# Performance work log

Measured on AMD Instinct MI355X. Metric: run time of the kernel, lower is better.

Reference implementation:

```python
import math
import jax, jax.numpy as jnp
import numpy as np

B, A, U, S, E, HYP, H = 16384, 32, 64, 2048, 32, 64, 4
ATTEND_REG_COEF = 1e-3


def setup_inputs() -> dict:
    key = jax.random.key(0)
    ks = jax.random.split(key, 12)
    sc = 0.05
    return {
        "agent_qs": jax.random.normal(ks[0], (B, A), jnp.float32),
        "states": jax.random.normal(ks[1], (B, S), jnp.float32),
        # per-head selector hypernet: Linear(S,HYP)+ReLU+Linear(HYP,E,no bias)
        "sel_w1": jax.random.normal(ks[2], (H, S, HYP), jnp.float32) * sc,
        "sel_b1": jax.random.normal(ks[3], (H, HYP), jnp.float32) * sc,
        "sel_w2": jax.random.normal(ks[4], (H, HYP, E), jnp.float32) * sc,
        # per-head key extractor: Linear(U,E,no bias)
        "key_w": jax.random.normal(ks[5], (H, U, E), jnp.float32) * sc,
        # V net: Linear(S,E)+ReLU+Linear(E,1)
        "v_w1": jax.random.normal(ks[6], (S, E), jnp.float32) * sc,
        "v_b1": jax.random.normal(ks[7], (E,), jnp.float32) * sc,
        "v_w2": jax.random.normal(ks[8], (E, 1), jnp.float32) * sc,
        "v_b2": jax.random.normal(ks[9], (1,), jnp.float32) * sc,
    }


def reference(agent_qs, states, sel_w1, sel_b1, sel_w2, key_w, v_w1, v_b1, v_w2, v_b2):
    # nonlinear=False, weighted_head=False, state_bias=True (defaults used here)
    unit_states = states[:, : A * U].reshape(-1, A, U)  # [B, A, U]

    # per-head selectors: [B, H, E]
    h1 = jax.nn.relu(jnp.einsum("bs,hsk->bhk", states, sel_w1) + sel_b1[None])
    selectors = jnp.einsum("bhk,hke->bhe", h1, sel_w2)

    # per-head, per-agent keys: [B, H, A, E]
    keys = jnp.einsum("bau,hue->bhae", unit_states, key_w)

    # attention logits [B, H, A] (matches selector @ stacked-keys in torch)
    logits = jnp.einsum("bhe,bhae->bha", selectors, keys)
    weights = jax.nn.softmax(logits / math.sqrt(E), axis=-1)  # [B, H, A]

    head_attend = jnp.sum(weights, axis=1)  # [B, A]

    v = jax.nn.relu(states @ v_w1 + v_b1) @ v_w2 + v_b2  # [B, 1]

    # coef * sum over heads of mean(logits_h ** 2)
    attend_mag_regs = ATTEND_REG_COEF * jnp.sum(jnp.mean(logits ** 2, axis=(0, 2)))

    # per-head entropy: -(p * log(p + 1e-8)).sum(agents).mean(batch) -> [H]
    head_entropies = -jnp.mean(
        jnp.sum(weights * jnp.log(weights + 1e-8), axis=-1), axis=0
    )

    return head_attend, v, attend_mag_regs, head_entropies
```

## Files before the change

### kernel.cpp

```cpp
#include <hip/hip_runtime.h>
#include <hip/hip_bf16.h>

#define B_N 16384
#define A_N 32
#define U_N 64
#define S_N 2048
#define E_N 32
#define HYP_N 64
#define H_N 4
#define NREAL 288
#define NPADG 320

#define H1B_STRIDE 264

#define WS_WT    0
#define WS_MB    1310720
#define WS_PMAG  (WS_MB + 32768)
#define WS_PENT  (WS_PMAG + 65536)
#define WS_T     (WS_PENT + 262144)
#define WS_HV    (WS_T + 16777216)

#define OUT_V   (B_N * A_N)
#define OUT_MAG (OUT_V + B_N)
#define OUT_ENT (OUT_MAG + 1)

typedef __attribute__((ext_vector_type(8))) short bf16x8_t;
typedef __attribute__((ext_vector_type(4))) float floatx4_t;

#define AS1(p) ((const __attribute__((address_space(1))) void*)(p))
#define AS3(p) ((__attribute__((address_space(3))) void*)(p))

__device__ __forceinline__ unsigned short f2b(float f) {
    union { float f; unsigned u; } v; v.f = f;
    unsigned r = v.u + 0x7FFFu + ((v.u >> 16) & 1u);
    return (unsigned short)(r >> 16);
}
__device__ __forceinline__ float b2f(unsigned x) {
    union { unsigned u; float f; } v; v.u = x << 16; return v.f;
}
__device__ __forceinline__ uint4 pack_bf16x8(float4 a0, float4 a1) {
    uint4 o;
    o.x = (unsigned)f2b(a0.x) | ((unsigned)f2b(a0.y) << 16);
    o.y = (unsigned)f2b(a0.z) | ((unsigned)f2b(a0.w) << 16);
    o.z = (unsigned)f2b(a1.x) | ((unsigned)f2b(a1.y) << 16);
    o.w = (unsigned)f2b(a1.z) | ((unsigned)f2b(a1.w) << 16);
    return o;
}

__global__ __launch_bounds__(256) void pack_w_kernel(
        const float* __restrict__ sel_w1, const float* __restrict__ v_w1,
        const float* __restrict__ sel_w2, const float* __restrict__ key_w,
        unsigned short* __restrict__ Wt, unsigned short* __restrict__ Mb) {
    int idx = blockIdx.x * 256 + threadIdx.x;
    if (idx < NPADG * S_N) {
        int n = idx >> 11;
        int k = idx & 2047;
        float val = 0.0f;
        if (n < 256) {
            int h = n >> 6, kk = n & 63;
            val = sel_w1[((size_t)h * S_N + k) * HYP_N + kk];
        } else if (n < NREAL) {
            val = v_w1[(size_t)k * E_N + (n - 256)];
        }
        Wt[idx] = f2b(val);
    } else if (idx < NPADG * S_N + H_N * U_N * HYP_N) {
        int j = idx - NPADG * S_N;
        int h = j >> 12, u = (j >> 6) & 63, k = j & 63;
        const float* kw = key_w + ((size_t)h * U_N + u) * E_N;
        const float* w2 = sel_w2 + ((size_t)h * HYP_N + k) * E_N;
        float s = 0.0f;
#pragma unroll
        for (int e = 0; e < E_N; ++e) s = fmaf(kw[e], w2[e], s);
        Mb[j] = f2b(s);
    }
}

#define FM_BM 32
#define FM_BK 64
#define NIT   (S_N / FM_BK)

__global__ __launch_bounds__(256, 3) void gemm_t_kernel(
        const float* __restrict__ states, const unsigned short* __restrict__ Wt,
        const float* __restrict__ sel_b1, const float* __restrict__ v_b1,
        const unsigned short* __restrict__ Mb,
        float* __restrict__ tg, unsigned short* __restrict__ hv) {
    __shared__ __align__(16) char pool[4096 + 40960];
    unsigned short* Asm = (unsigned short*)pool;
    unsigned short* Bsm = (unsigned short*)(pool + 4096);
    unsigned short* h1b = (unsigned short*)pool;

    const int t = threadIdx.x;
    const int lane = t & 63;
    const int w = t >> 6;
    const int m0 = blockIdx.x * FM_BM;
    const int nw = w * 80;

    const int ar = t >> 3, acl = t & 7;
    const float* ap = states + (size_t)(m0 + ar) * S_N + acl * 8;
    const int aph = acl ^ (ar & 7);

    floatx4_t acc[2][5] = {};
    float4 a0, a1;

    a0 = *(const float4*)(ap);
    a1 = *(const float4*)(ap + 4);
    *(uint4*)(Asm + (size_t)(ar * 8 + aph) * 8) = pack_bf16x8(a0, a1);
#pragma unroll
    for (int i = 0; i < 10; ++i) {
        int p = i * 256 + t, n = p >> 3, sl = p & 7;
        int cl = sl ^ (n & 7);
        __builtin_amdgcn_global_load_lds(AS1(Wt + (size_t)n * S_N + cl * 8),
                                         AS3(Bsm + p * 8), 16, 0, 0);
    }
    a0 = *(const float4*)(ap + FM_BK);
    a1 = *(const float4*)(ap + FM_BK + 4);
    __syncthreads();

    for (int it = 0; it < NIT; ++it) {
#pragma unroll
        for (int s = 0; s < 2; ++s) {
            const int c = s * 4 + (lane >> 4);
            bf16x8_t afr[2];
#pragma unroll
            for (int mt = 0; mt < 2; ++mt) {
                int r = mt * 16 + (lane & 15);
                afr[mt] = *(const bf16x8_t*)(Asm + r * 64 + (c ^ (r & 7)) * 8);
            }
#pragma unroll
            for (int nt = 0; nt < 5; ++nt) {
                int n = nw + nt * 16 + (lane & 15);
                bf16x8_t bfr = *(const bf16x8_t*)(Bsm + n * 64 + (c ^ (n & 7)) * 8);
                acc[0][nt] = __builtin_amdgcn_mfma_f32_16x16x32_bf16(
                    afr[0], bfr, acc[0][nt], 0, 0, 0);
                acc[1][nt] = __builtin_amdgcn_mfma_f32_16x16x32_bf16(
                    afr[1], bfr, acc[1][nt], 0, 0, 0);
            }
        }
        __syncthreads();
        if (it < NIT - 1) {
            int k0 = (it + 1) * FM_BK;
            *(uint4*)(Asm + (size_t)(ar * 8 + aph) * 8) = pack_bf16x8(a0, a1);
#pragma unroll
            for (int i = 0; i < 10; ++i) {
                int p = i * 256 + t, n = p >> 3, sl = p & 7;
                int cl = sl ^ (n & 7);
                __builtin_amdgcn_global_load_lds(
                    AS1(Wt + (size_t)n * S_N + k0 + cl * 8),
                    AS3(Bsm + p * 8), 16, 0, 0);
            }
            if (it < NIT - 2) {
                const float* g = ap + (it + 2) * FM_BK;
                a0 = *(const float4*)(g);
                a1 = *(const float4*)(g + 4);
            }
            __syncthreads();
        }
    }

#pragma unroll
    for (int nt = 0; nt < 5; ++nt) {
        int n = nw + nt * 16 + (lane & 15);
        if (n < 256) {
            float bias = sel_b1[n];
#pragma unroll
            for (int mt = 0; mt < 2; ++mt)
#pragma unroll
                for (int rg = 0; rg < 4; ++rg) {
                    int r = mt * 16 + (lane >> 4) * 4 + rg;
                    float v = acc[mt][nt][rg] + bias;
                    h1b[r * H1B_STRIDE + n] = f2b(v > 0.0f ? v : 0.0f);
                }
        } else if (n < NREAL) {
            int j = n - 256;
            float bias = v_b1[j];
#pragma unroll
            for (int mt = 0; mt < 2; ++mt)
#pragma unroll
                for (int rg = 0; rg < 4; ++rg) {
                    int r = mt * 16 + (lane >> 4) * 4 + rg;
                    float v = acc[mt][nt][rg] + bias;
                    hv[(size_t)(m0 + r) * 32 + j] = f2b(v > 0.0f ? v : 0.0f);
                }
        }
    }
    __syncthreads();

    {
        const int h = w;
        floatx4_t tacc[2][4] = {};
#pragma unroll
        for (int s = 0; s < 2; ++s) {
            int k0 = s * 32 + (lane >> 4) * 8;
            bf16x8_t afr[2];
#pragma unroll
            for (int mt = 0; mt < 2; ++mt)
                afr[mt] = *(const bf16x8_t*)(
                    h1b + (mt * 16 + (lane & 15)) * H1B_STRIDE + h * 64 + k0);
#pragma unroll
            for (int ut = 0; ut < 4; ++ut) {
                int u = ut * 16 + (lane & 15);
                bf16x8_t bfr = *(const bf16x8_t*)(Mb + ((size_t)(h * U_N + u) * 64) + k0);
#pragma unroll
                for (int mt = 0; mt < 2; ++mt)
                    tacc[mt][ut] = __builtin_amdgcn_mfma_f32_16x16x32_bf16(
                        afr[mt], bfr, tacc[mt][ut], 0, 0, 0);
            }
        }
#pragma unroll
        for (int mt = 0; mt < 2; ++mt)
#pragma unroll
            for (int ut = 0; ut < 4; ++ut)
#pragma unroll
                for (int rg = 0; rg < 4; ++rg) {
                    int b = m0 + mt * 16 + (lane >> 4) * 4 + rg;
                    int u = ut * 16 + (lane & 15);
                    tg[((size_t)b * H_N + h) * U_N + u] = tacc[mt][ut][rg];
                }
    }
}

#define L_BM 16

__global__ __launch_bounds__(256, 8) void attend_l_kernel(
        const float* __restrict__ states, const float* __restrict__ tg,
        const unsigned short* __restrict__ hv,
        const float* __restrict__ v_w2, const float* __restrict__ v_b2,
        float* __restrict__ out, float* __restrict__ pmag, float* __restrict__ pent) {
    const int t = threadIdx.x;
    const int lane = t & 63;
    const int w = t >> 6;
    const int m0 = blockIdx.x * L_BM;
    const int a = lane & 31, uh = lane >> 5;

    for (int rr = 0; rr < 4; ++rr) {
        const int b = m0 + w * 4 + rr;
        const float* up = states + (size_t)b * S_N + a * 64 + uh * 32;
        const float* tp = tg + (size_t)b * (H_N * U_N) + uh * 32;
        float pl[4] = {0.0f, 0.0f, 0.0f, 0.0f};
        float4 c0 = ((const float4*)up)[0];
        float4 c1 = ((const float4*)up)[1];
#pragma unroll
        for (int i = 0; i < 8; ++i) {
            float4 s4 = c0;
            c0 = c1;
            if (i < 6) c1 = ((const float4*)up)[i + 2];
#pragma unroll
            for (int h = 0; h < 4; ++h) {
                float4 t4 = *(const float4*)(tp + h * U_N + i * 4);
                pl[h] = fmaf(s4.x, t4.x, pl[h]);
                pl[h] = fmaf(s4.y, t4.y, pl[h]);
                pl[h] = fmaf(s4.z, t4.z, pl[h]);
                pl[h] = fmaf(s4.w, t4.w, pl[h]);
            }
        }
#pragma unroll
        for (int h = 0; h < 4; ++h)
            pl[h] += __shfl_xor(pl[h], 32, 64);

        float mg = pl[0]*pl[0] + pl[1]*pl[1] + pl[2]*pl[2] + pl[3]*pl[3];
#pragma unroll
        for (int o = 16; o > 0; o >>= 1) mg += __shfl_xor(mg, o, 32);

        float hatt = 0.0f;
        float entv[4];
#pragma unroll
        for (int h = 0; h < 4; ++h) {
            float x = pl[h] * 0.17677669529663687f;
            float p = __expf(x);
            float den = p, px = p * x;
#pragma unroll
            for (int o = 16; o > 0; o >>= 1) {
                den += __shfl_xor(den, o, 32);
                px  += __shfl_xor(px,  o, 32);
            }
            float inv = 1.0f / den;
            hatt = fmaf(p, inv, hatt);
            entv[h] = px * inv - __logf(den);
        }

        if (uh == 0) {
            out[(size_t)b * A_N + a] = hatt;
            float pv = b2f((unsigned)hv[(size_t)b * 32 + a]) * v_w2[a];
#pragma unroll
            for (int o = 16; o > 0; o >>= 1) pv += __shfl_xor(pv, o, 32);
            if (a == 0) {
                out[OUT_V + b] = pv + v_b2[0];
                pmag[b] = mg;
#pragma unroll
                for (int h = 0; h < 4; ++h) pent[(size_t)h * B_N + b] = entv[h];
            }
        }
    }
}

__global__ __launch_bounds__(256) void finalize_kernel(
        const float* __restrict__ pmag, const float* __restrict__ pent,
        float* __restrict__ out) {
    int which = blockIdx.x;
    const float* src = (which == 0) ? pmag : (pent + (size_t)(which - 1) * B_N);
    float s = 0.0f;
    for (int i = threadIdx.x; i < B_N; i += 256) s += src[i];
#pragma unroll
    for (int o = 32; o > 0; o >>= 1) s += __shfl_xor(s, o, 64);
    __shared__ float red[4];
    if ((threadIdx.x & 63) == 0) red[threadIdx.x >> 6] = s;
    __syncthreads();
    if (threadIdx.x == 0) {
        float tot = red[0] + red[1] + red[2] + red[3];
        if (which == 0) out[OUT_MAG] = 1e-3f * tot / (float)(B_N * A_N);
        else out[OUT_ENT + which - 1] = -tot / (float)B_N;
    }
}

extern "C" void kernel_launch(void* const* d_in, const int* in_sizes, int n_in,
                              void* d_out, int out_size, void* d_ws, size_t ws_size,
                              hipStream_t stream) {
    const float* states = (const float*)d_in[1];
    const float* sel_w1 = (const float*)d_in[2];
    const float* sel_b1 = (const float*)d_in[3];
    const float* sel_w2 = (const float*)d_in[4];
    const float* key_w  = (const float*)d_in[5];
    const float* v_w1   = (const float*)d_in[6];
    const float* v_b1   = (const float*)d_in[7];
    const float* v_w2   = (const float*)d_in[8];
    const float* v_b2   = (const float*)d_in[9];
    float* out = (float*)d_out;
    char* wsb  = (char*)d_ws;

    unsigned short* Wt  = (unsigned short*)(wsb + WS_WT);
    unsigned short* Mb  = (unsigned short*)(wsb + WS_MB);
    float* pmag         = (float*)(wsb + WS_PMAG);
    float* pent         = (float*)(wsb + WS_PENT);
    float* tg           = (float*)(wsb + WS_T);
    unsigned short* hv  = (unsigned short*)(wsb + WS_HV);

    pack_w_kernel<<<dim3((NPADG * S_N + H_N * U_N * HYP_N + 255) / 256),
                    dim3(256), 0, stream>>>(sel_w1, v_w1, sel_w2, key_w, Wt, Mb);
    gemm_t_kernel<<<dim3(B_N / FM_BM), dim3(256), 0, stream>>>(
        states, Wt, sel_b1, v_b1, Mb, tg, hv);
    attend_l_kernel<<<dim3(B_N / L_BM), dim3(256), 0, stream>>>(
        states, tg, hv, v_w2, v_b2, out, pmag, pent);
    finalize_kernel<<<dim3(5), dim3(256), 0, stream>>>(pmag, pent, out);
}
```

Measured before the change: 306.2 us.

## Load B operand directly to registers with double-buffered A tile in LDS

The weight (B) operand no longer goes through LDS. Each wave loads its own B fragments from global memory straight into a double-buffered register set (bX/bY), one k-step ahead. The A tile is double-buffered in LDS, which needs only one barrier per iteration instead of two, and LDS shrinks to the h1b epilogue size. This removes the LDS staging and the barrier stall for B, but costs many more VGPRs (occupancy hint lowered from 3 to 2 blocks) and relies on L2 to absorb the redundant B reads across blocks.

```diff
diff --git a/kernel.cpp b/kernel.cpp
--- a/kernel.cpp
+++ b/kernel.cpp
@@ -79,14 +79,50 @@
 #define FM_BK 64
 #define NIT   (S_N / FM_BK)
 
-__global__ __launch_bounds__(256, 3) void gemm_t_kernel(
+#define GEMM_BODY(T, BC, BN, CB, NB)                                         \
+    {                                                                        \
+        const int tt = (T);                                                  \
+        if (tt < NIT - 1)                                                    \
+            *(uint4*)(Asm + (NB) + (ar * 8 + aph) * 8) = pack_bf16x8(a0, a1);\
+        if (tt < NIT - 2) {                                                  \
+            const float* g = ap + (tt + 2) * FM_BK;                          \
+            a0 = *(const float4*)(g);                                        \
+            a1 = *(const float4*)(g + 4);                                    \
+        }                                                                    \
+        if (tt < NIT - 1) {                                                  \
+            const int k0 = (tt + 1) * FM_BK;                                 \
+            _Pragma("unroll")                                                \
+            for (int s = 0; s < 2; ++s)                                      \
+                _Pragma("unroll")                                            \
+                for (int nt = 0; nt < 5; ++nt)                               \
+                    BN[s * 5 + nt] = *(const bf16x8_t*)(                     \
+                        bb + (size_t)nt * 16 * S_N + k0 + s * 32);           \
+        }                                                                    \
+        _Pragma("unroll")                                                    \
+        for (int s = 0; s < 2; ++s) {                                        \
+            const int c = s * 4 + q;                                         \
+            const int ph = (c ^ (r & 7)) * 8;                                \
+            bf16x8_t af0 = *(const bf16x8_t*)(Asm + (CB) + r * 64 + ph);     \
+            bf16x8_t af1 = *(const bf16x8_t*)(Asm + (CB) + (16 + r) * 64 + ph);\
+            _Pragma("unroll")                                                \
+            for (int nt = 0; nt < 5; ++nt) {                                 \
+                acc[0][nt] = __builtin_amdgcn_mfma_f32_16x16x32_bf16(        \
+                    af0, BC[s * 5 + nt], acc[0][nt], 0, 0, 0);               \
+                acc[1][nt] = __builtin_amdgcn_mfma_f32_16x16x32_bf16(        \
+                    af1, BC[s * 5 + nt], acc[1][nt], 0, 0, 0);               \
+            }                                                                \
+        }                                                                    \
+        asm volatile("s_waitcnt lgkmcnt(0)" ::: "memory");                   \
+        __builtin_amdgcn_s_barrier();                                        \
+    }
+
+__global__ __launch_bounds__(256, 2) void gemm_t_kernel(
         const float* __restrict__ states, const unsigned short* __restrict__ Wt,
         const float* __restrict__ sel_b1, const float* __restrict__ v_b1,
         const unsigned short* __restrict__ Mb,
         float* __restrict__ tg, unsigned short* __restrict__ hv) {
-    __shared__ __align__(16) char pool[4096 + 40960];
+    __shared__ __align__(16) char pool[H1B_STRIDE * FM_BM * 2];
     unsigned short* Asm = (unsigned short*)pool;
-    unsigned short* Bsm = (unsigned short*)(pool + 4096);
     unsigned short* h1b = (unsigned short*)pool;
 
     const int t = threadIdx.x;
@@ -94,67 +130,35 @@
     const int w = t >> 6;
     const int m0 = blockIdx.x * FM_BM;
     const int nw = w * 80;
+    const int q = lane >> 4, r = lane & 15;
 
     const int ar = t >> 3, acl = t & 7;
     const float* ap = states + (size_t)(m0 + ar) * S_N + acl * 8;
     const int aph = acl ^ (ar & 7);
 
+    const unsigned short* bb = Wt + (size_t)(nw + r) * S_N + q * 8;
+
     floatx4_t acc[2][5] = {};
     float4 a0, a1;
+    bf16x8_t bX[10], bY[10];
 
     a0 = *(const float4*)(ap);
     a1 = *(const float4*)(ap + 4);
-    *(uint4*)(Asm + (size_t)(ar * 8 + aph) * 8) = pack_bf16x8(a0, a1);
-#pragma unroll
-    for (int i = 0; i < 10; ++i) {
-        int p = i * 256 + t, n = p >> 3, sl = p & 7;
-        int cl = sl ^ (n & 7);
-        __builtin_amdgcn_global_load_lds(AS1(Wt + (size_t)n * S_N + cl * 8),
-                                         AS3(Bsm + p * 8), 16, 0, 0);
-    }
+#pragma unroll
+    for (int s = 0; s < 2; ++s)
+#pragma unroll
+        for (int nt = 0; nt < 5; ++nt)
+            bX[s * 5 + nt] = *(const bf16x8_t*)(
+                bb + (size_t)nt * 16 * S_N + s * 32);
+    *(uint4*)(Asm + (ar * 8 + aph) * 8) = pack_bf16x8(a0, a1);
     a0 = *(const float4*)(ap + FM_BK);
     a1 = *(const float4*)(ap + FM_BK + 4);
-    __syncthreads();
-
-    for (int it = 0; it < NIT; ++it) {
-#pragma unroll
-        for (int s = 0; s < 2; ++s) {
-            const int c = s * 4 + (lane >> 4);
-            bf16x8_t afr[2];
-#pragma unroll
-            for (int mt = 0; mt < 2; ++mt) {
-                int r = mt * 16 + (lane & 15);
-                afr[mt] = *(const bf16x8_t*)(Asm + r * 64 + (c ^ (r & 7)) * 8);
-            }
-#pragma unroll
-            for (int nt = 0; nt < 5; ++nt) {
-                int n = nw + nt * 16 + (lane & 15);
-                bf16x8_t bfr = *(const bf16x8_t*)(Bsm + n * 64 + (c ^ (n & 7)) * 8);
-                acc[0][nt] = __builtin_amdgcn_mfma_f32_16x16x32_bf16(
-                    afr[0], bfr, acc[0][nt], 0, 0, 0);
-                acc[1][nt] = __builtin_amdgcn_mfma_f32_16x16x32_bf16(
-                    afr[1], bfr, acc[1][nt], 0, 0, 0);
-            }
-        }
-        __syncthreads();
-        if (it < NIT - 1) {
-            int k0 = (it + 1) * FM_BK;
-            *(uint4*)(Asm + (size_t)(ar * 8 + aph) * 8) = pack_bf16x8(a0, a1);
-#pragma unroll
-            for (int i = 0; i < 10; ++i) {
-                int p = i * 256 + t, n = p >> 3, sl = p & 7;
-                int cl = sl ^ (n & 7);
-                __builtin_amdgcn_global_load_lds(
-                    AS1(Wt + (size_t)n * S_N + k0 + cl * 8),
-                    AS3(Bsm + p * 8), 16, 0, 0);
-            }
-            if (it < NIT - 2) {
-                const float* g = ap + (it + 2) * FM_BK;
-                a0 = *(const float4*)(g);
-                a1 = *(const float4*)(g + 4);
-            }
-            __syncthreads();
-        }
+    asm volatile("s_waitcnt lgkmcnt(0)" ::: "memory");
+    __builtin_amdgcn_s_barrier();
+
+    for (int it2 = 0; it2 < NIT / 2; ++it2) {
+        GEMM_BODY(it2 * 2,     bX, bY, 0,    2048);
+        GEMM_BODY(it2 * 2 + 1, bY, bX, 2048, 0);
     }
 
 #pragma unroll
@@ -166,9 +170,9 @@
             for (int mt = 0; mt < 2; ++mt)
 #pragma unroll
                 for (int rg = 0; rg < 4; ++rg) {
-                    int r = mt * 16 + (lane >> 4) * 4 + rg;
+                    int rr = mt * 16 + (lane >> 4) * 4 + rg;
                     float v = acc[mt][nt][rg] + bias;
-                    h1b[r * H1B_STRIDE + n] = f2b(v > 0.0f ? v : 0.0f);
+                    h1b[rr * H1B_STRIDE + n] = f2b(v > 0.0f ? v : 0.0f);
                 }
         } else if (n < NREAL) {
             int j = n - 256;
@@ -177,9 +181,9 @@
             for (int mt = 0; mt < 2; ++mt)
 #pragma unroll
                 for (int rg = 0; rg < 4; ++rg) {
-                    int r = mt * 16 + (lane >> 4) * 4 + rg;
+                    int rr = mt * 16 + (lane >> 4) * 4 + rg;
                     float v = acc[mt][nt][rg] + bias;
-                    hv[(size_t)(m0 + r) * 32 + j] = f2b(v > 0.0f ? v : 0.0f);
+                    hv[(size_t)(m0 + rr) * 32 + j] = f2b(v > 0.0f ? v : 0.0f);
                 }
         }
     }
```

Result: slower. 339.1 us (+10.7%).

## Split GEMM N-dimension across block pairs and load A fragments directly to registers

Applied to the files above, without the earlier changes.

The fused states×weights GEMM now uses 64-row M tiles with 512-thread blocks. Each pair of blocks splits the N dimension: one block handles columns 0-191 (heads 0-2) and the other columns 192-287 (head 3 plus the V hidden layer). The previous kernel computed padded columns up to 320, and this split drops them. The A operand is converted from fp32 to bf16 in registers and fed straight to MFMA, skipping the LDS staging, and LDS use per block shrinks. The cost is that the two blocks of a pair each read the same states rows from global memory, and the second block has less work, so load is unbalanced.

```diff
diff --git a/kernel.cpp b/kernel.cpp
--- a/kernel.cpp
+++ b/kernel.cpp
@@ -11,8 +11,6 @@
 #define NREAL 288
 #define NPADG 320
 
-#define H1B_STRIDE 264
-
 #define WS_WT    0
 #define WS_MB    1310720
 #define WS_PMAG  (WS_MB + 32768)
@@ -38,13 +36,13 @@
 __device__ __forceinline__ float b2f(unsigned x) {
     union { unsigned u; float f; } v; v.u = x << 16; return v.f;
 }
-__device__ __forceinline__ uint4 pack_bf16x8(float4 a0, float4 a1) {
-    uint4 o;
-    o.x = (unsigned)f2b(a0.x) | ((unsigned)f2b(a0.y) << 16);
-    o.y = (unsigned)f2b(a0.z) | ((unsigned)f2b(a0.w) << 16);
-    o.z = (unsigned)f2b(a1.x) | ((unsigned)f2b(a1.y) << 16);
-    o.w = (unsigned)f2b(a1.z) | ((unsigned)f2b(a1.w) << 16);
-    return o;
+__device__ __forceinline__ bf16x8_t cvt_a8(float4 a0, float4 a1) {
+    union { uint4 u; bf16x8_t v; } cv;
+    cv.u.x = (unsigned)f2b(a0.x) | ((unsigned)f2b(a0.y) << 16);
+    cv.u.y = (unsigned)f2b(a0.z) | ((unsigned)f2b(a0.w) << 16);
+    cv.u.z = (unsigned)f2b(a1.x) | ((unsigned)f2b(a1.y) << 16);
+    cv.u.w = (unsigned)f2b(a1.z) | ((unsigned)f2b(a1.w) << 16);
+    return cv.v;
 }
 
 __global__ __launch_bounds__(256) void pack_w_kernel(
@@ -75,148 +73,166 @@
     }
 }
 
-#define FM_BM 32
+#define FM_BM 64
 #define FM_BK 64
 #define NIT   (S_N / FM_BK)
-
-__global__ __launch_bounds__(256, 3) void gemm_t_kernel(
+#define H1B_ST 200
+#define POOL_B 25600
+
+template<int PART>
+__device__ __forceinline__ void gemm_body(
+        const float* __restrict__ states, const unsigned short* __restrict__ Wt,
+        const float* __restrict__ sel_b1, const float* __restrict__ v_b1,
+        const unsigned short* __restrict__ Mb,
+        float* __restrict__ tg, unsigned short* __restrict__ hv,
+        unsigned short* Bsm, unsigned short* h1b) {
+    constexpr int NT2   = PART ? 3 : 6;
+    constexpr int NROW  = PART ? 96 : 192;
+    constexpr int NBASE = PART ? 192 : 0;
+    constexpr int NGR   = NROW * 8;
+
+    const int t = threadIdx.x;
+    const int lane = t & 63;
+    const int w = t >> 6;
+    const int m0 = (int)(blockIdx.x >> 1) * FM_BM;
+    const int mq = w >> 1;
+    const int nh = w & 1;
+    const int q = lane >> 4, r = lane & 15;
+
+    const float* ap = states + (size_t)(m0 + mq * 16 + r) * S_N + q * 8;
+
+    floatx4_t acc[NT2] = {};
+    float4 aC0, aC1, aC2, aC3;
+
+#pragma unroll
+    for (int i = 0; i < 3; ++i) {
+        int p = i * 512 + t;
+        if (PART == 0 || p < NGR) {
+            int n = p >> 3, sl = p & 7;
+            int cl = sl ^ (n & 7);
+            __builtin_amdgcn_global_load_lds(
+                AS1(Wt + (size_t)(NBASE + n) * S_N + cl * 8),
+                AS3(Bsm + (size_t)p * 8), 16, 0, 0);
+        }
+    }
+    aC0 = *(const float4*)(ap);
+    aC1 = *(const float4*)(ap + 4);
+    aC2 = *(const float4*)(ap + 32);
+    aC3 = *(const float4*)(ap + 36);
+    __syncthreads();
+
+    for (int it = 0; it < NIT; ++it) {
+        bf16x8_t af0 = cvt_a8(aC0, aC1);
+        bf16x8_t af1 = cvt_a8(aC2, aC3);
+#pragma unroll
+        for (int s = 0; s < 2; ++s) {
+            const int c = s * 4 + q;
+            bf16x8_t af = s ? af1 : af0;
+#pragma unroll
+            for (int j = 0; j < NT2; ++j) {
+                int n = (nh * NT2 + j) * 16 + r;
+                bf16x8_t bfr = *(const bf16x8_t*)(
+                    Bsm + n * 64 + ((c ^ (n & 7)) * 8));
+                acc[j] = __builtin_amdgcn_mfma_f32_16x16x32_bf16(
+                    af, bfr, acc[j], 0, 0, 0);
+            }
+        }
+        __syncthreads();
+        if (it < NIT - 1) {
+            const float* g = ap + (it + 1) * FM_BK;
+            aC0 = *(const float4*)(g);
+            aC1 = *(const float4*)(g + 4);
+            aC2 = *(const float4*)(g + 32);
+            aC3 = *(const float4*)(g + 36);
+            int k0 = (it + 1) * FM_BK;
+#pragma unroll
+            for (int i = 0; i < 3; ++i) {
+                int p = i * 512 + t;
+                if (PART == 0 || p < NGR) {
+                    int n = p >> 3, sl = p & 7;
+                    int cl = sl ^ (n & 7);
+                    __builtin_amdgcn_global_load_lds(
+                        AS1(Wt + (size_t)(NBASE + n) * S_N + k0 + cl * 8),
+                        AS3(Bsm + (size_t)p * 8), 16, 0, 0);
+                }
+            }
+            __syncthreads();
+        }
+    }
+
+#pragma unroll
+    for (int j = 0; j < NT2; ++j) {
+        int lc = (nh * NT2 + j) * 16 + r;
+        int n = NBASE + lc;
+        if (n < 256) {
+            float bias = sel_b1[n];
+#pragma unroll
+            for (int rg = 0; rg < 4; ++rg) {
+                int rr = mq * 16 + q * 4 + rg;
+                float v = acc[j][rg] + bias;
+                h1b[rr * H1B_ST + lc] = f2b(v > 0.0f ? v : 0.0f);
+            }
+        } else {
+            float bias = v_b1[n - 256];
+#pragma unroll
+            for (int rg = 0; rg < 4; ++rg) {
+                int rr = mq * 16 + q * 4 + rg;
+                float v = acc[j][rg] + bias;
+                hv[(size_t)(m0 + rr) * 32 + (n - 256)] = f2b(v > 0.0f ? v : 0.0f);
+            }
+        }
+    }
+    __syncthreads();
+
+    if (PART ? (w < 2) : (w < 6)) {
+        const int h = PART ? 3 : (w >> 1);
+        const int rb = (PART ? w : (w & 1)) * 32;
+        const int lcb = h * 64 - NBASE;
+        floatx4_t tacc[2][4] = {};
+#pragma unroll
+        for (int s = 0; s < 2; ++s) {
+            int k0 = s * 32 + q * 8;
+            bf16x8_t afr[2];
+#pragma unroll
+            for (int mt = 0; mt < 2; ++mt)
+                afr[mt] = *(const bf16x8_t*)(
+                    h1b + (rb + mt * 16 + r) * H1B_ST + lcb + k0);
+#pragma unroll
+            for (int ut = 0; ut < 4; ++ut) {
+                int u = ut * 16 + r;
+                bf16x8_t bfr = *(const bf16x8_t*)(
+                    Mb + ((size_t)(h * U_N + u) * 64) + k0);
+#pragma unroll
+                for (int mt = 0; mt < 2; ++mt)
+                    tacc[mt][ut] = __builtin_amdgcn_mfma_f32_16x16x32_bf16(
+                        afr[mt], bfr, tacc[mt][ut], 0, 0, 0);
+            }
+        }
+#pragma unroll
+        for (int mt = 0; mt < 2; ++mt)
+#pragma unroll
+            for (int ut = 0; ut < 4; ++ut)
+#pragma unroll
+                for (int rg = 0; rg < 4; ++rg) {
+                    int b = m0 + rb + mt * 16 + q * 4 + rg;
+                    int u = ut * 16 + r;
+                    tg[((size_t)b * H_N + h) * U_N + u] = tacc[mt][ut][rg];
+                }
+    }
+}
+
+__global__ __launch_bounds__(512, 4) void gemm_t_kernel(
         const float* __restrict__ states, const unsigned short* __restrict__ Wt,
         const float* __restrict__ sel_b1, const float* __restrict__ v_b1,
         const unsigned short* __restrict__ Mb,
         float* __restrict__ tg, unsigned short* __restrict__ hv) {
-    __shared__ __align__(16) char pool[4096 + 40960];
-    unsigned short* Asm = (unsigned short*)pool;
-    unsigned short* Bsm = (unsigned short*)(pool + 4096);
+    __shared__ __align__(16) char pool[POOL_B];
+    unsigned short* Bsm = (unsigned short*)pool;
     unsigned short* h1b = (unsigned short*)pool;
-
-    const int t = threadIdx.x;
-    const int lane = t & 63;
-    const int w = t >> 6;
-    const int m0 = blockIdx.x * FM_BM;
-    const int nw = w * 80;
-
-    const int ar = t >> 3, acl = t & 7;
-    const float* ap = states + (size_t)(m0 + ar) * S_N + acl * 8;
-    const int aph = acl ^ (ar & 7);
-
-    floatx4_t acc[2][5] = {};
-    float4 a0, a1;
-
-    a0 = *(const float4*)(ap);
-    a1 = *(const float4*)(ap + 4);
-    *(uint4*)(Asm + (size_t)(ar * 8 + aph) * 8) = pack_bf16x8(a0, a1);
-#pragma unroll
-    for (int i = 0; i < 10; ++i) {
-        int p = i * 256 + t, n = p >> 3, sl = p & 7;
-        int cl = sl ^ (n & 7);
-        __builtin_amdgcn_global_load_lds(AS1(Wt + (size_t)n * S_N + cl * 8),
-                                         AS3(Bsm + p * 8), 16, 0, 0);
-    }
-    a0 = *(const float4*)(ap + FM_BK);
-    a1 = *(const float4*)(ap + FM_BK + 4);
-    __syncthreads();
-
-    for (int it = 0; it < NIT; ++it) {
-#pragma unroll
-        for (int s = 0; s < 2; ++s) {
-            const int c = s * 4 + (lane >> 4);
-            bf16x8_t afr[2];
-#pragma unroll
-            for (int mt = 0; mt < 2; ++mt) {
-                int r = mt * 16 + (lane & 15);
-                afr[mt] = *(const bf16x8_t*)(Asm + r * 64 + (c ^ (r & 7)) * 8);
-            }
-#pragma unroll
-            for (int nt = 0; nt < 5; ++nt) {
-                int n = nw + nt * 16 + (lane & 15);
-                bf16x8_t bfr = *(const bf16x8_t*)(Bsm + n * 64 + (c ^ (n & 7)) * 8);
-                acc[0][nt] = __builtin_amdgcn_mfma_f32_16x16x32_bf16(
-                    afr[0], bfr, acc[0][nt], 0, 0, 0);
-                acc[1][nt] = __builtin_amdgcn_mfma_f32_16x16x32_bf16(
-                    afr[1], bfr, acc[1][nt], 0, 0, 0);
-            }
-        }
-        __syncthreads();
-        if (it < NIT - 1) {
-            int k0 = (it + 1) * FM_BK;
-            *(uint4*)(Asm + (size_t)(ar * 8 + aph) * 8) = pack_bf16x8(a0, a1);
-#pragma unroll
-            for (int i = 0; i < 10; ++i) {
-                int p = i * 256 + t, n = p >> 3, sl = p & 7;
-                int cl = sl ^ (n & 7);
-                __builtin_amdgcn_global_load_lds(
-                    AS1(Wt + (size_t)n * S_N + k0 + cl * 8),
-                    AS3(Bsm + p * 8), 16, 0, 0);
-            }
-            if (it < NIT - 2) {
-                const float* g = ap + (it + 2) * FM_BK;
-                a0 = *(const float4*)(g);
-                a1 = *(const float4*)(g + 4);
-            }
-            __syncthreads();
-        }
-    }
-
-#pragma unroll
-    for (int nt = 0; nt < 5; ++nt) {
-        int n = nw + nt * 16 + (lane & 15);
-        if (n < 256) {
-            float bias = sel_b1[n];
-#pragma unroll
-            for (int mt = 0; mt < 2; ++mt)
-#pragma unroll
-                for (int rg = 0; rg < 4; ++rg) {
-                    int r = mt * 16 + (lane >> 4) * 4 + rg;
-                    float v = acc[mt][nt][rg] + bias;
-                    h1b[r * H1B_STRIDE + n] = f2b(v > 0.0f ? v : 0.0f);
-                }
-        } else if (n < NREAL) {
-            int j = n - 256;
-            float bias = v_b1[j];
-#pragma unroll
-            for (int mt = 0; mt < 2; ++mt)
-#pragma unroll
-                for (int rg = 0; rg < 4; ++rg) {
-                    int r = mt * 16 + (lane >> 4) * 4 + rg;
-                    float v = acc[mt][nt][rg] + bias;
-                    hv[(size_t)(m0 + r) * 32 + j] = f2b(v > 0.0f ? v : 0.0f);
-                }
-        }
-    }
-    __syncthreads();
-
-    {
-        const int h = w;
-        floatx4_t tacc[2][4] = {};
-#pragma unroll
-        for (int s = 0; s < 2; ++s) {
-            int k0 = s * 32 + (lane >> 4) * 8;
-            bf16x8_t afr[2];
-#pragma unroll
-            for (int mt = 0; mt < 2; ++mt)
-                afr[mt] = *(const bf16x8_t*)(
-                    h1b + (mt * 16 + (lane & 15)) * H1B_STRIDE + h * 64 + k0);
-#pragma unroll
-            for (int ut = 0; ut < 4; ++ut) {
-                int u = ut * 16 + (lane & 15);
-                bf16x8_t bfr = *(const bf16x8_t*)(Mb + ((size_t)(h * U_N + u) * 64) + k0);
-#pragma unroll
-                for (int mt = 0; mt < 2; ++mt)
-                    tacc[mt][ut] = __builtin_amdgcn_mfma_f32_16x16x32_bf16(
-                        afr[mt], bfr, tacc[mt][ut], 0, 0, 0);
-            }
-        }
-#pragma unroll
-        for (int mt = 0; mt < 2; ++mt)
-#pragma unroll
-            for (int ut = 0; ut < 4; ++ut)
-#pragma unroll
-                for (int rg = 0; rg < 4; ++rg) {
-                    int b = m0 + mt * 16 + (lane >> 4) * 4 + rg;
-                    int u = ut * 16 + (lane & 15);
-                    tg[((size_t)b * H_N + h) * U_N + u] = tacc[mt][ut][rg];
-                }
-    }
+    if ((blockIdx.x & 1) == 0)
+        gemm_body<0>(states, Wt, sel_b1, v_b1, Mb, tg, hv, Bsm, h1b);
+    else
+        gemm_body<1>(states, Wt, sel_b1, v_b1, Mb, tg, hv, Bsm, h1b);
 }
 
 #define L_BM 16
@@ -336,7 +352,7 @@
 
     pack_w_kernel<<<dim3((NPADG * S_N + H_N * U_N * HYP_N + 255) / 256),
                     dim3(256), 0, stream>>>(sel_w1, v_w1, sel_w2, key_w, Wt, Mb);
-    gemm_t_kernel<<<dim3(B_N / FM_BM), dim3(256), 0, stream>>>(
+    gemm_t_kernel<<<dim3(2 * (B_N / FM_BM)), dim3(512), 0, stream>>>(
         states, Wt, sel_b1, v_b1, Mb, tg, hv);
     attend_l_kernel<<<dim3(B_N / L_BM), dim3(256), 0, stream>>>(
         states, tg, hv, v_w2, v_b2, out, pmag, pent);
```

Result: slower. 325.2 us (+6.2%).
